# Kernel tuning notes

Measured on AMD Instinct MI355X. Metric: run time of the kernel, lower is better.

Reference implementation:

```python
import jax, jax.numpy as jnp
import numpy as np

T, B, D, H, O = 128, 256, 512, 1024, 1


def setup_inputs() -> dict:
    key = jax.random.key(0)
    ks = jax.random.split(key, 10)
    s_in = 1.0 / np.sqrt(D)
    s_h = 1.0 / np.sqrt(H)
    u = lambda k, shape, s: jax.random.uniform(k, shape, jnp.float32, -s, s)
    return {
        "inputs": jax.random.normal(ks[0], (T, B, D), jnp.float32),
        "hidden_state": jnp.zeros((1, B, H), jnp.float32),
        "cell_state": jnp.zeros((1, B, H), jnp.float32),
        "W1": u(ks[1], (H, D), s_in),
        "b1": u(ks[2], (H,), s_in),
        "W_ih": u(ks[3], (4 * H, H), s_h),
        "W_hh": u(ks[4], (4 * H, H), s_h),
        "b_ih": u(ks[5], (4 * H,), s_h),
        "b_hh": u(ks[6], (4 * H,), s_h),
        "W_out": u(ks[7], (O, H), s_h),
        "b_out": u(ks[8], (O,), s_h),
    }


def reference(inputs, hidden_state, cell_state, W1, b1, W_ih, W_hh, b_ih, b_hh, W_out, b_out):
    # first_layer + ReLU (dropout is identity in eval mode)
    x = jax.nn.relu(jnp.einsum("tbd,hd->tbh", inputs, W1) + b1)  # (T,B,H)
    # Precompute input contribution to all gates for every timestep.
    xg = jnp.einsum("tbh,gh->tbg", x, W_ih) + b_ih + b_hh  # (T,B,4H)
    h0 = hidden_state[0]
    c0 = cell_state[0]

    def step(carry, xg_t):
        h, c = carry
        g = xg_t + h @ W_hh.T  # (B,4H), PyTorch gate order i,f,g,o
        i, f, gg, o = jnp.split(g, 4, axis=-1)
        i = jax.nn.sigmoid(i)
        f = jax.nn.sigmoid(f)
        gg = jnp.tanh(gg)
        o = jax.nn.sigmoid(o)
        c = f * c + i * gg
        h = o * jnp.tanh(c)
        return (h, c), h

    (hT, cT), hs = jax.lax.scan(step, (h0, c0), xg)
    out = jnp.einsum("tbh,oh->tbo", hs, W_out) + b_out  # (T,B,O)
    return out, hT[None], cT[None]
```

## Files before the change

### kernel.cpp

```cpp
#include <hip/hip_runtime.h>
#include <hip/hip_bf16.h>
#include <math.h>


#define T_STEPS 128
#define BATCH   256
#define DIM     512
#define HID     1024
#define GATES   4096
#define FPAD    32

typedef __attribute__((ext_vector_type(8))) short short8;
typedef __attribute__((ext_vector_type(4))) float f4;
typedef __attribute__((ext_vector_type(4))) int i4;

__device__ __forceinline__ short f2bf(float f) {
    union { float f; unsigned u; } x; x.f = f;
    unsigned r = (x.u + 0x7fffu + ((x.u >> 16) & 1u)) >> 16;
    return (short)r;
}
__device__ __forceinline__ float bf2f(short s) {
    union { unsigned u; float f; } x; x.u = ((unsigned)(unsigned short)s) << 16;
    return x.f;
}
__device__ __forceinline__ float sigm(float x) { return 1.f / (1.f + __expf(-x)); }
__device__ __forceinline__ float tanh_fast(float x) { return 2.f / (1.f + __expf(-2.f * x)) - 1.f; }

__device__ __forceinline__ void gll16(const void* g, void* l) {
    __builtin_amdgcn_global_load_lds(
        (const __attribute__((address_space(1))) void*)g,
        (__attribute__((address_space(3))) void*)l, 16, 0, 0);
}
__device__ __forceinline__ void store16_wt(void* p, i4 v) {
    asm volatile("global_store_dwordx4 %0, %1, off sc0 sc1"
                 :: "v"(p), "v"(v) : "memory");
}

__global__ __launch_bounds__(256) void cvt_f32_bf16(const float* __restrict__ in,
                                                    short* __restrict__ out, int n4) {
    int i = blockIdx.x * 256 + threadIdx.x;
    if (i < n4) {
        float4 v = ((const float4*)in)[i];
        union { short s[4]; long long ll; } r;
        r.s[0] = f2bf(v.x); r.s[1] = f2bf(v.y); r.s[2] = f2bf(v.z); r.s[3] = f2bf(v.w);
        ((long long*)out)[i] = r.ll;
    }
}

__global__ __launch_bounds__(256) void cvt_h0_blocked(const float* __restrict__ h0,
                                                      short* __restrict__ dst) {
    int b = blockIdx.x, k0 = threadIdx.x * 4;
    float4 v = *(const float4*)&h0[(size_t)b * HID + k0];
    union { short s[4]; long long ll; } p;
    p.s[0] = f2bf(v.x); p.s[1] = f2bf(v.y); p.s[2] = f2bf(v.z); p.s[3] = f2bf(v.w);
    *(long long*)&dst[(k0 >> 3) * (BATCH * 8) + b * 8 + (k0 & 7)] = p.ll;
}

__global__ __launch_bounds__(256) void cvt_permute_rows(const float* __restrict__ in,
                                                        short* __restrict__ out) {
    int r = blockIdx.x;
    int hc = r >> 2, g = r & 3;
    const float* src = in + (size_t)(g * HID + hc) * HID;
    short* dst = out + (size_t)r * HID;
    int c = threadIdx.x * 4;
    float4 v = *(const float4*)&src[c];
    union { short s[4]; long long ll; } p;
    p.s[0] = f2bf(v.x); p.s[1] = f2bf(v.y); p.s[2] = f2bf(v.z); p.s[3] = f2bf(v.w);
    *(long long*)&dst[c] = p.ll;
}

__global__ __launch_bounds__(256) void bias_sum_perm(const float* __restrict__ a,
                                                     const float* __restrict__ b,
                                                     float* __restrict__ o) {
    int r = blockIdx.x * 256 + threadIdx.x;
    int hc = r >> 2, g = r & 3;
    int src = g * HID + hc;
    o[r] = a[src] + b[src];
}

__global__ __launch_bounds__(256) void copy_f32v4(const float* __restrict__ in,
                                                  float* __restrict__ out, int n4) {
    int i = blockIdx.x * 256 + threadIdx.x;
    if (i < n4) ((float4*)out)[i] = ((const float4*)in)[i];
}

__global__ __launch_bounds__(256) void zero_i32(int* __restrict__ p, int n) {
    for (int i = blockIdx.x * 256 + threadIdx.x; i < n; i += gridDim.x * 256)
        p[i] = 0;
}

__global__ __launch_bounds__(512) void gemm_bt8(const short* __restrict__ A,
                                                const short* __restrict__ B,
                                                const float* __restrict__ bias,
                                                short* __restrict__ C,
                                                int M, int N, int K, int do_relu) {
    __shared__ __align__(16) short As[2][256 * 64];
    __shared__ __align__(16) short Bs[2][256 * 64];
    const int tid = threadIdx.x, w = tid >> 6, lane = tid & 63;
    const int wr = w >> 2, wc = w & 3;

    const int nwg = gridDim.x * gridDim.y;
    const int flat = blockIdx.y * gridDim.x + blockIdx.x;
    const int qq = nwg >> 3, rr = nwg & 7;
    const int xcd = flat & 7, oin = flat >> 3;
    const int swz = (xcd < rr ? xcd * (qq + 1) : rr * (qq + 1) + (xcd - rr) * qq) + oin;
    const int bm = (swz % gridDim.x) * 256, bn = (swz / gridDim.x) * 256;

    const int NT = K >> 6, NI = NT >> 1;

#define STG(P, L, bmn, kt, h)                                                  \
    if ((kt) < NT) {                                                           \
        _Pragma("unroll")                                                      \
        for (int s_ = 0; s_ < 2; ++s_) {                                       \
            int r0_ = (h) * 128 + s_ * 64 + w * 8;                             \
            int row_ = r0_ + (lane >> 3);                                      \
            int kof_ = ((lane & 7) ^ (row_ & 7)) * 8;                          \
            gll16(&P[(size_t)((bmn) + row_) * K + (kt) * 64 + kof_],           \
                  &L[(kt) & 1][r0_ * 64]);                                     \
        }                                                                      \
    }

#define LOADB(kt)                                                              \
    _Pragma("unroll")                                                          \
    for (int nf = 0; nf < 4; ++nf)                                             \
        _Pragma("unroll")                                                      \
        for (int ks = 0; ks < 2; ++ks) {                                       \
            int rb_ = wc * 64 + nf * 16 + (lane & 15);                         \
            int sb_ = (ks * 4 + (lane >> 4)) ^ (rb_ & 7);                      \
            bfr[nf][ks] = *(const short8*)&Bs[(kt) & 1][rb_ * 64 + sb_ * 8];   \
        }

#define LOADA(kt, q)                                                           \
    _Pragma("unroll")                                                          \
    for (int mi = 0; mi < 2; ++mi)                                             \
        _Pragma("unroll")                                                      \
        for (int ks = 0; ks < 2; ++ks) {                                       \
            int ra_ = wr * 128 + ((q) * 2 + mi) * 16 + (lane & 15);            \
            int sa_ = (ks * 4 + (lane >> 4)) ^ (ra_ & 7);                      \
            af[mi][ks] = *(const short8*)&As[(kt) & 1][ra_ * 64 + sa_ * 8];    \
        }

#define MFMAQ(q)                                                               \
    __builtin_amdgcn_s_setprio(1);                                             \
    _Pragma("unroll")                                                          \
    for (int mi = 0; mi < 2; ++mi)                                             \
        _Pragma("unroll")                                                      \
        for (int nf = 0; nf < 4; ++nf)                                         \
            _Pragma("unroll")                                                  \
            for (int ks = 0; ks < 2; ++ks)                                     \
                acc[(q) * 2 + mi][nf] = __builtin_amdgcn_mfma_f32_16x16x32_bf16( \
                    af[mi][ks], bfr[nf][ks], acc[(q) * 2 + mi][nf], 0, 0, 0);  \
    __builtin_amdgcn_s_setprio(0);                                             \
    __builtin_amdgcn_sched_barrier(0);

#define VM4 asm volatile("s_waitcnt vmcnt(4)" ::: "memory");
#define VM0 asm volatile("s_waitcnt vmcnt(0)" ::: "memory");
#define BAR __builtin_amdgcn_s_barrier();

    f4 acc[8][4] = {};

    STG(A, As, bm, 0, 0) STG(A, As, bm, 0, 1)
    STG(B, Bs, bn, 0, 0) STG(B, Bs, bn, 0, 1)
    STG(B, Bs, bn, 1, 0) STG(B, Bs, bn, 1, 1)

    for (int it = 0; it < NI; ++it) {
        const int kt0 = 2 * it, kt1 = 2 * it + 1;
        const int lastit = (it + 1 == NI);
        short8 bfr[4][2], af[2][2];

        VM4 BAR
        LOADB(kt0) LOADA(kt0, 0)
        STG(A, As, bm, kt1, 0)
        MFMAQ(0)
        BAR
        LOADA(kt0, 1)
        STG(A, As, bm, kt1, 1)
        MFMAQ(1)
        BAR
        LOADA(kt0, 2)
        STG(B, Bs, bn, kt0 + 2, 0)
        MFMAQ(2)
        BAR
        LOADA(kt0, 3)
        STG(B, Bs, bn, kt0 + 2, 1)
        MFMAQ(3)

        if (lastit) { VM0 } else { VM4 }
        BAR
        LOADB(kt1) LOADA(kt1, 0)
        STG(A, As, bm, kt0 + 2, 0)
        MFMAQ(0)
        BAR
        LOADA(kt1, 1)
        STG(A, As, bm, kt0 + 2, 1)
        MFMAQ(1)
        BAR
        LOADA(kt1, 2)
        STG(B, Bs, bn, kt1 + 2, 0)
        MFMAQ(2)
        BAR
        LOADA(kt1, 3)
        STG(B, Bs, bn, kt1 + 2, 1)
        MFMAQ(3)
    }
#undef STG
#undef LOADB
#undef LOADA
#undef MFMAQ
#undef VM4
#undef VM0
#undef BAR

    const int lc = lane & 15, lr = (lane >> 4) * 4;
#pragma unroll
    for (int mf = 0; mf < 8; ++mf) {
#pragma unroll
        for (int nf = 0; nf < 4; ++nf) {
            int col = bn + wc * 64 + nf * 16 + lc;
            float bv = bias[col];
#pragma unroll
            for (int r = 0; r < 4; ++r) {
                int row = bm + wr * 128 + mf * 16 + lr + r;
                float v = acc[mf][nf][r] + bv;
                if (do_relu) v = fmaxf(v, 0.f);
                C[(size_t)row * N + col] = f2bf(v);
            }
        }
    }
}

__global__ __launch_bounds__(256) void lstm_persist(const short* __restrict__ Whh,
                                                    const short* __restrict__ xgc,
                                                    short* __restrict__ hist,
                                                    float* __restrict__ cf,
                                                    float* __restrict__ hT,
                                                    float* __restrict__ cT,
                                                    int* __restrict__ flags,
                                                    int* __restrict__ go,
                                                    int TC, int last) {
    __shared__ __align__(16) short Bf[32768];
    __shared__ __align__(16) short Ht[512];
    const int tid = threadIdx.x, w = tid >> 6, lane = tid & 63;
    const int bg = blockIdx.x >> 7, cg = blockIdx.x & 127;
    const int bb = bg * 64, hc0 = cg * 8;
    const int hcl = lane & 7, gp = (lane >> 3) & 1, q = lane >> 4;

#pragma unroll
    for (int i = 0; i < 16; ++i) {
        int p = w * 16 + i;
        int c = p >> 1, t = p & 1;
        gll16(&Whh[(size_t)((t * 2 + gp) * HID + hc0 + hcl) * HID + c * 32 + q * 8],
              &Bf[p * 512]);
    }

    const int rowb = bb + w * 16 + q * 4 + gp * 2;
    float creg[2];
#pragma unroll
    for (int e = 0; e < 2; ++e)
        creg[e] = cf[(size_t)(rowb + e) * HID + hc0 + hcl];

    __syncthreads();

    unsigned long long xw[2], xwn[2];
#pragma unroll
    for (int e = 0; e < 2; ++e)
        xw[e] = *(const unsigned long long*)&xgc[(size_t)(rowb + e) * GATES
                                                 + (hc0 + hcl) * 4];

#define ISSUE_A(buf, g)                                                        \
    _Pragma("unroll")                                                          \
    for (int i = 0; i < 8; ++i)                                                \
        buf[i] = *(const short8*)(abase + (size_t)((g) * 8 + i) * astr);

#define COMPUTE_A(buf, g)                                                      \
    __builtin_amdgcn_s_setprio(1);                                             \
    _Pragma("unroll")                                                          \
    for (int i = 0; i < 8; ++i) {                                              \
        short8 b0 = *(const short8*)&Bf[(((g) * 8 + i) * 2 + 0) * 512 + lane * 8]; \
        short8 b1 = *(const short8*)&Bf[(((g) * 8 + i) * 2 + 1) * 512 + lane * 8]; \
        acc0 = __builtin_amdgcn_mfma_f32_16x16x32_bf16(buf[i], b0, acc0, 0, 0, 0); \
        acc1 = __builtin_amdgcn_mfma_f32_16x16x32_bf16(buf[i], b1, acc1, 0, 0, 0); \
    }                                                                          \
    __builtin_amdgcn_s_setprio(0);

    for (int tt = 0; tt < TC; ++tt) {
        if (tt + 1 < TC) {
#pragma unroll
            for (int e = 0; e < 2; ++e)
                xwn[e] = *(const unsigned long long*)&xgc[(size_t)((tt + 1) * BATCH + rowb + e) * GATES
                                                          + (hc0 + hcl) * 4];
        }

        const short* abase = hist + (size_t)tt * BATCH * HID
                           + (size_t)q * (BATCH * 8) + (size_t)(bb + w * 16 + (lane & 15)) * 8;
        const size_t astr = (size_t)4 * (BATCH * 8);
        f4 acc0 = {}, acc1 = {};
        short8 ab0[8], ab1[8], ab2[8];
        ISSUE_A(ab0, 0)
        ISSUE_A(ab1, 1)
        ISSUE_A(ab2, 2)
        COMPUTE_A(ab0, 0)
        ISSUE_A(ab0, 3)
        COMPUTE_A(ab1, 1)
        COMPUTE_A(ab2, 2)
        COMPUTE_A(ab0, 3)

        float p0[4], p1[4];
#pragma unroll
        for (int r = 0; r < 4; ++r) {
            p0[r] = __shfl_xor(acc0[r], 8);
            p1[r] = __shfl_xor(acc1[r], 8);
        }

        int glast = last && (tt == TC - 1);
#pragma unroll
        for (int e = 0; e < 2; ++e) {
            int r = gp * 2 + e;
            size_t b = rowb + e;
            float gi = gp ? p0[r] : acc0[r];
            float gf = gp ? acc0[r] : p0[r];
            float gg = gp ? p1[r] : acc1[r];
            float go_ = gp ? acc1[r] : p1[r];
            gi += bf2f((short)(xw[e] & 0xffff));
            gf += bf2f((short)((xw[e] >> 16) & 0xffff));
            gg += bf2f((short)((xw[e] >> 32) & 0xffff));
            go_ += bf2f((short)((xw[e] >> 48) & 0xffff));
            float si = sigm(gi), sf = sigm(gf), tg = tanh_fast(gg), so = sigm(go_);
            float cn = sf * creg[e] + si * tg;
            float hv = so * tanh_fast(cn);
            creg[e] = cn;
            Ht[(w * 16 + q * 4 + gp * 2 + e) * 8 + hcl] = f2bf(hv);
            if (glast) {
                hT[b * HID + hc0 + hcl] = hv;
                cT[b * HID + hc0 + hcl] = cn;
            }
        }
        xw[0] = xwn[0]; xw[1] = xwn[1];
        __syncthreads();

        short* hn = hist + (size_t)(tt + 1) * BATCH * HID
                  + (size_t)cg * (BATCH * 8) + (size_t)bb * 8;
        if (tid < 64)
            store16_wt(&hn[tid * 8], *(const i4*)&Ht[tid * 8]);

        if (tt < TC - 1) {
            __syncthreads();
            const int base = (tt * 4 + bg) * 128 * FPAD;
            if (tid == 0)
                __hip_atomic_store(&flags[base + cg * FPAD], 1,
                                   __ATOMIC_RELAXED, __HIP_MEMORY_SCOPE_AGENT);
            if (cg == 0) {
                if (tid < 128) {
                    while (__hip_atomic_load(&flags[base + tid * FPAD],
                                             __ATOMIC_RELAXED, __HIP_MEMORY_SCOPE_AGENT) == 0)
                        __builtin_amdgcn_s_sleep(1);
                }
                __syncthreads();
                if (tid == 0)
                    __hip_atomic_store(&go[(tt * 4 + bg) * FPAD], 1,
                                       __ATOMIC_RELAXED, __HIP_MEMORY_SCOPE_AGENT);
            } else {
                if (tid == 0) {
                    while (__hip_atomic_load(&go[(tt * 4 + bg) * FPAD],
                                             __ATOMIC_RELAXED, __HIP_MEMORY_SCOPE_AGENT) == 0)
                        __builtin_amdgcn_s_sleep(1);
                }
                __syncthreads();
            }
        }
    }

#undef ISSUE_A
#undef COMPUTE_A

#pragma unroll
    for (int e = 0; e < 2; ++e)
        cf[(size_t)(rowb + e) * HID + hc0 + hcl] = creg[e];
}

__global__ __launch_bounds__(256) void out_head(const short* __restrict__ hs,
                                                const float* __restrict__ Wout,
                                                const float* __restrict__ bout,
                                                float* __restrict__ out) {
    int row = blockIdx.x * 4 + (threadIdx.x >> 6);
    int lane = threadIdx.x & 63;
    int tt = row >> 8, b = row & 255;
    const short* sb = hs + (size_t)(tt + 1) * BATCH * HID + b * 8;
    const float2* w2 = (const float2*)Wout;
    float s = 0.f;
#pragma unroll
    for (int j = 0; j < 8; ++j) {
        int m = j * 64 + lane;
        int pk = *(const int*)&sb[(size_t)(m >> 2) * (BATCH * 8) + 2 * (m & 3)];
        float2 wv = w2[m];
        union { unsigned u; float f; } lo, hi;
        lo.u = ((unsigned)pk) << 16;
        hi.u = ((unsigned)pk) & 0xffff0000u;
        s += lo.f * wv.x + hi.f * wv.y;
    }
#pragma unroll
    for (int off = 32; off; off >>= 1) s += __shfl_down(s, off);
    if (lane == 0) out[row] = s + bout[0];
}

extern "C" void kernel_launch(void* const* d_in, const int* in_sizes, int n_in,
                              void* d_out, int out_size, void* d_ws, size_t ws_size,
                              hipStream_t stream) {
    const float* inputs = (const float*)d_in[0];
    const float* h0     = (const float*)d_in[1];
    const float* c0     = (const float*)d_in[2];
    const float* W1     = (const float*)d_in[3];
    const float* b1     = (const float*)d_in[4];
    const float* W_ih   = (const float*)d_in[5];
    const float* W_hh   = (const float*)d_in[6];
    const float* b_ih   = (const float*)d_in[7];
    const float* b_hh   = (const float*)d_in[8];
    const float* W_out  = (const float*)d_in[9];
    const float* b_out  = (const float*)d_in[10];

    float* out = (float*)d_out;
    float* hT  = out + (size_t)T_STEPS * BATCH;
    float* cT  = hT + (size_t)BATCH * HID;

    char* base = (char*)d_ws;
    size_t off = 0;
    auto alloc = [&](size_t bytes) -> char* {
        char* q = base + off;
        off += (bytes + 255) & ~(size_t)255;
        return q;
    };
    short* W1b   = (short*)alloc((size_t)HID * DIM * 2);
    short* Wihb  = (short*)alloc((size_t)GATES * HID * 2);
    short* Whhb  = (short*)alloc((size_t)GATES * HID * 2);
    float* biasf = (float*)alloc((size_t)GATES * 4);
    float* cf    = (float*)alloc((size_t)BATCH * HID * 4);
    int*   flags = (int*)alloc((size_t)T_STEPS * 4 * 128 * FPAD * 4);
    int*   go    = (int*)alloc((size_t)T_STEPS * 4 * FPAD * 4);

    short* xb_a  = (short*)alloc((size_t)T_STEPS * BATCH * HID * 2);
    short* hhist = (short*)alloc((size_t)(T_STEPS + 1) * BATCH * HID * 2);

    size_t xg_all_bytes = (size_t)T_STEPS * BATCH * GATES * 2;
    size_t inb_bytes    = (size_t)T_STEPS * BATCH * DIM * 2;
    int ALLX = (ws_size - off) >= (xg_all_bytes + 4096);
    short *xgb = nullptr, *inb_a = nullptr;
    int TC = 32;
    if (ALLX) {
        xgb   = (short*)alloc(xg_all_bytes);
        inb_a = xgb;
    } else {
        size_t per_c = (size_t)TC * BATCH * GATES * 2;
        while (TC > 1 && off + (per_c > inb_bytes ? per_c : inb_bytes) + 4096 > ws_size) {
            TC >>= 1;
            per_c = (size_t)TC * BATCH * GATES * 2;
        }
        size_t region = per_c > inb_bytes ? per_c : inb_bytes;
        xgb   = (short*)alloc(region);
        inb_a = xgb;
    }

    cvt_f32_bf16<<<(HID * DIM / 4 + 255) / 256, 256, 0, stream>>>(W1, W1b, HID * DIM / 4);
    cvt_permute_rows<<<GATES, 256, 0, stream>>>(W_ih, Wihb);
    cvt_f32_bf16<<<(GATES * HID / 4 + 255) / 256, 256, 0, stream>>>(W_hh, Whhb, GATES * HID / 4);
    bias_sum_perm<<<GATES / 256, 256, 0, stream>>>(b_ih, b_hh, biasf);
    cvt_h0_blocked<<<BATCH, 256, 0, stream>>>(h0, hhist);
    copy_f32v4<<<(BATCH * HID / 4 + 255) / 256, 256, 0, stream>>>(c0, cf, BATCH * HID / 4);
    zero_i32<<<512, 256, 0, stream>>>(flags, T_STEPS * 4 * 128 * FPAD + T_STEPS * 4 * FPAD);

    {
        int Ma = T_STEPS * BATCH;
        cvt_f32_bf16<<<(Ma * DIM / 4 + 255) / 256, 256, 0, stream>>>(
            inputs, inb_a, Ma * DIM / 4);
        gemm_bt8<<<dim3(Ma / 256, HID / 256), 512, 0, stream>>>(
            inb_a, W1b, b1, xb_a, Ma, HID, DIM, 1);
        if (ALLX) {
            gemm_bt8<<<dim3(Ma / 256, GATES / 256), 512, 0, stream>>>(
                xb_a, Wihb, biasf, xgb, Ma, GATES, HID, 0);
        }
    }

    for (int t0 = 0; t0 < T_STEPS; t0 += TC) {
        int last = (t0 + TC >= T_STEPS);
        const short* xgc;
        if (ALLX) {
            xgc = xgb + (size_t)t0 * BATCH * GATES;
        } else {
            int Mc = TC * BATCH;
            gemm_bt8<<<dim3(Mc / 256, GATES / 256), 512, 0, stream>>>(
                xb_a + (size_t)t0 * BATCH * HID, Wihb, biasf, xgb,
                Mc, GATES, HID, 0);
            xgc = xgb;
        }

        lstm_persist<<<512, 256, 0, stream>>>(Whhb, xgc,
                                              hhist + (size_t)t0 * BATCH * HID,
                                              cf, hT, cT,
                                              flags + (size_t)t0 * 4 * 128 * FPAD,
                                              go + (size_t)t0 * 4 * FPAD,
                                              TC, last);
    }

    out_head<<<T_STEPS * BATCH / 4, 256, 0, stream>>>(hhist, W_out, b_out, out);
}
```

Before: 1.166 ms.

## Fuse prep kernels into one launch, read c0 directly, lighten per-step barrier

Merges the weight, input and h0 conversions, the bias sum and the flag zeroing into a single prep_all launch. It drops the c0 copy by having the first LSTM launch read c0 directly. It also replaces the per-step __syncthreads before the flag store with a vmcnt wait done only in wave 0. This cuts launch overhead and shortens the per-timestep sync in the persistent loop. The catch is that other waves' write-through stores of h may no longer be ordered before the flag is published, which risks a race.

```diff
diff --git a/kernel.cpp b/kernel.cpp
--- a/kernel.cpp
+++ b/kernel.cpp
@@ -35,58 +35,63 @@
     asm volatile("global_store_dwordx4 %0, %1, off sc0 sc1"
                  :: "v"(p), "v"(v) : "memory");
 }
-
-__global__ __launch_bounds__(256) void cvt_f32_bf16(const float* __restrict__ in,
-                                                    short* __restrict__ out, int n4) {
-    int i = blockIdx.x * 256 + threadIdx.x;
-    if (i < n4) {
-        float4 v = ((const float4*)in)[i];
-        union { short s[4]; long long ll; } r;
-        r.s[0] = f2bf(v.x); r.s[1] = f2bf(v.y); r.s[2] = f2bf(v.z); r.s[3] = f2bf(v.w);
-        ((long long*)out)[i] = r.ll;
-    }
-}
-
-__global__ __launch_bounds__(256) void cvt_h0_blocked(const float* __restrict__ h0,
-                                                      short* __restrict__ dst) {
-    int b = blockIdx.x, k0 = threadIdx.x * 4;
-    float4 v = *(const float4*)&h0[(size_t)b * HID + k0];
-    union { short s[4]; long long ll; } p;
-    p.s[0] = f2bf(v.x); p.s[1] = f2bf(v.y); p.s[2] = f2bf(v.z); p.s[3] = f2bf(v.w);
-    *(long long*)&dst[(k0 >> 3) * (BATCH * 8) + b * 8 + (k0 & 7)] = p.ll;
-}
-
-__global__ __launch_bounds__(256) void cvt_permute_rows(const float* __restrict__ in,
-                                                        short* __restrict__ out) {
-    int r = blockIdx.x;
-    int hc = r >> 2, g = r & 3;
-    const float* src = in + (size_t)(g * HID + hc) * HID;
-    short* dst = out + (size_t)r * HID;
-    int c = threadIdx.x * 4;
-    float4 v = *(const float4*)&src[c];
-    union { short s[4]; long long ll; } p;
-    p.s[0] = f2bf(v.x); p.s[1] = f2bf(v.y); p.s[2] = f2bf(v.z); p.s[3] = f2bf(v.w);
-    *(long long*)&dst[c] = p.ll;
-}
-
-__global__ __launch_bounds__(256) void bias_sum_perm(const float* __restrict__ a,
-                                                     const float* __restrict__ b,
-                                                     float* __restrict__ o) {
-    int r = blockIdx.x * 256 + threadIdx.x;
-    int hc = r >> 2, g = r & 3;
-    int src = g * HID + hc;
-    o[r] = a[src] + b[src];
-}
-
-__global__ __launch_bounds__(256) void copy_f32v4(const float* __restrict__ in,
-                                                  float* __restrict__ out, int n4) {
-    int i = blockIdx.x * 256 + threadIdx.x;
-    if (i < n4) ((float4*)out)[i] = ((const float4*)in)[i];
-}
-
-__global__ __launch_bounds__(256) void zero_i32(int* __restrict__ p, int n) {
-    for (int i = blockIdx.x * 256 + threadIdx.x; i < n; i += gridDim.x * 256)
-        p[i] = 0;
+__device__ __forceinline__ void cvt4(const float* src, short* dst, int i) {
+    float4 v = ((const float4*)src)[i];
+    union { short s[4]; long long ll; } r;
+    r.s[0] = f2bf(v.x); r.s[1] = f2bf(v.y); r.s[2] = f2bf(v.z); r.s[3] = f2bf(v.w);
+    ((long long*)dst)[i] = r.ll;
+}
+
+#define PREP_BLOCKS 25872
+__global__ __launch_bounds__(256) void prep_all(const float* __restrict__ inputs,
+                                                const float* __restrict__ W1,
+                                                const float* __restrict__ W_ih,
+                                                const float* __restrict__ W_hh,
+                                                const float* __restrict__ b_ih,
+                                                const float* __restrict__ b_hh,
+                                                const float* __restrict__ h0,
+                                                short* __restrict__ inb,
+                                                short* __restrict__ W1b,
+                                                short* __restrict__ Wihb,
+                                                short* __restrict__ Whhb,
+                                                float* __restrict__ biasf,
+                                                short* __restrict__ h0dst,
+                                                int* __restrict__ flags,
+                                                int nflags) {
+    int bx = blockIdx.x;
+    const int tid = threadIdx.x;
+    if (bx < 16384) {
+        cvt4(inputs, inb, bx * 256 + tid);
+    } else if ((bx -= 16384) < 512) {
+        cvt4(W1, W1b, bx * 256 + tid);
+    } else if ((bx -= 512) < 4096) {
+        int r = bx;
+        int hc = r >> 2, g = r & 3;
+        const float* src = W_ih + (size_t)(g * HID + hc) * HID;
+        short* dst = Wihb + (size_t)r * HID;
+        int c = tid * 4;
+        float4 v = *(const float4*)&src[c];
+        union { short s[4]; long long ll; } p;
+        p.s[0] = f2bf(v.x); p.s[1] = f2bf(v.y); p.s[2] = f2bf(v.z); p.s[3] = f2bf(v.w);
+        *(long long*)&dst[c] = p.ll;
+    } else if ((bx -= 4096) < 4096) {
+        cvt4(W_hh, Whhb, bx * 256 + tid);
+    } else if ((bx -= 4096) < 16) {
+        int r = bx * 256 + tid;
+        int hc = r >> 2, g = r & 3;
+        int src = g * HID + hc;
+        biasf[r] = b_ih[src] + b_hh[src];
+    } else if ((bx -= 16) < 256) {
+        int b = bx, k0 = tid * 4;
+        float4 v = *(const float4*)&h0[(size_t)b * HID + k0];
+        union { short s[4]; long long ll; } p;
+        p.s[0] = f2bf(v.x); p.s[1] = f2bf(v.y); p.s[2] = f2bf(v.z); p.s[3] = f2bf(v.w);
+        *(long long*)&h0dst[(k0 >> 3) * (BATCH * 8) + b * 8 + (k0 & 7)] = p.ll;
+    } else {
+        bx -= 256;
+        for (int i = bx * 256 + tid; i < nflags; i += 512 * 256)
+            flags[i] = 0;
+    }
 }
 
 __global__ __launch_bounds__(512) void gemm_bt8(const short* __restrict__ A,
@@ -232,6 +237,7 @@
 __global__ __launch_bounds__(256) void lstm_persist(const short* __restrict__ Whh,
                                                     const short* __restrict__ xgc,
                                                     short* __restrict__ hist,
+                                                    const float* __restrict__ cfin,
                                                     float* __restrict__ cf,
                                                     float* __restrict__ hT,
                                                     float* __restrict__ cT,
@@ -257,7 +263,7 @@
     float creg[2];
 #pragma unroll
     for (int e = 0; e < 2; ++e)
-        creg[e] = cf[(size_t)(rowb + e) * HID + hc0 + hcl];
+        creg[e] = cfin[(size_t)(rowb + e) * HID + hc0 + hcl];
 
     __syncthreads();
 
@@ -344,11 +350,13 @@
             store16_wt(&hn[tid * 8], *(const i4*)&Ht[tid * 8]);
 
         if (tt < TC - 1) {
-            __syncthreads();
             const int base = (tt * 4 + bg) * 128 * FPAD;
-            if (tid == 0)
-                __hip_atomic_store(&flags[base + cg * FPAD], 1,
-                                   __ATOMIC_RELAXED, __HIP_MEMORY_SCOPE_AGENT);
+            if (w == 0) {
+                asm volatile("s_waitcnt vmcnt(0)" ::: "memory");
+                if (tid == 0)
+                    __hip_atomic_store(&flags[base + cg * FPAD], 1,
+                                       __ATOMIC_RELAXED, __HIP_MEMORY_SCOPE_AGENT);
+            }
             if (cg == 0) {
                 if (tid < 128) {
                     while (__hip_atomic_load(&flags[base + tid * FPAD],
@@ -459,18 +467,13 @@
         inb_a = xgb;
     }
 
-    cvt_f32_bf16<<<(HID * DIM / 4 + 255) / 256, 256, 0, stream>>>(W1, W1b, HID * DIM / 4);
-    cvt_permute_rows<<<GATES, 256, 0, stream>>>(W_ih, Wihb);
-    cvt_f32_bf16<<<(GATES * HID / 4 + 255) / 256, 256, 0, stream>>>(W_hh, Whhb, GATES * HID / 4);
-    bias_sum_perm<<<GATES / 256, 256, 0, stream>>>(b_ih, b_hh, biasf);
-    cvt_h0_blocked<<<BATCH, 256, 0, stream>>>(h0, hhist);
-    copy_f32v4<<<(BATCH * HID / 4 + 255) / 256, 256, 0, stream>>>(c0, cf, BATCH * HID / 4);
-    zero_i32<<<512, 256, 0, stream>>>(flags, T_STEPS * 4 * 128 * FPAD + T_STEPS * 4 * FPAD);
+    prep_all<<<PREP_BLOCKS, 256, 0, stream>>>(
+        inputs, W1, W_ih, W_hh, b_ih, b_hh, h0,
+        inb_a, W1b, Wihb, Whhb, biasf, hhist, flags,
+        T_STEPS * 4 * 128 * FPAD + T_STEPS * 4 * FPAD);
 
     {
         int Ma = T_STEPS * BATCH;
-        cvt_f32_bf16<<<(Ma * DIM / 4 + 255) / 256, 256, 0, stream>>>(
-            inputs, inb_a, Ma * DIM / 4);
         gemm_bt8<<<dim3(Ma / 256, HID / 256), 512, 0, stream>>>(
             inb_a, W1b, b1, xb_a, Ma, HID, DIM, 1);
         if (ALLX) {
@@ -494,7 +497,7 @@
 
         lstm_persist<<<512, 256, 0, stream>>>(Whhb, xgc,
                                               hhist + (size_t)t0 * BATCH * HID,
-                                              cf, hT, cT,
+                                              (t0 == 0) ? c0 : cf, cf, hT, cT,
                                               flags + (size_t)t0 * 4 * 128 * FPAD,
                                               go + (size_t)t0 * 4 * FPAD,
                                               TC, last);
```

Result: no change. 1.183 ms (+1.4%).
